# Kernel tuning notes

Hardware: AMD Instinct MI355X
Metric: run time of the kernel (lower is better)

Reference implementation:

```python
import jax, jax.numpy as jnp
import numpy as np

LLR_CLIP = 20.0   # allowed_llr_range(abs=20)
QMAX = 7.5        # decoder_qms_qbit = 5 -> round(x*2)/2, clip +/-7.5


def _quantize_ste(x):
    # straight-through quantizer: forward = quantized, grad flows through clipped x
    q = jnp.clip(jnp.round(x * 2.0) / 2.0, -QMAX, QMAX)
    xc = jnp.clip(x, -QMAX, QMAX)
    return xc + jax.lax.stop_gradient(q - xc)


def _decode(xa, cn_weights, vn_idx, cn_idx, shifts, M):
    # xa: (B, Z, N) channel LLRs; messages live on lifted edges (B, Z, E)
    B, Z, N = xa.shape
    E = vn_idx.shape[0]
    iters = cn_weights.shape[0]

    zidx = jnp.arange(Z)
    lift = (zidx[:, None] + shifts[None, :]) % Z    # VN-domain -> CN-domain cyclic shift per edge
    unlift = (zidx[:, None] - shifts[None, :]) % Z  # inverse shift
    lift_b = jnp.broadcast_to(lift[None], (B, Z, E))
    unlift_b = jnp.broadcast_to(unlift[None], (B, Z, E))

    V = jax.nn.one_hot(vn_idx, N, dtype=xa.dtype)   # (E, N) edge->VN incidence (= W_output / W_skipconn2even)
    eids = jnp.arange(E)
    llr_e = xa[:, :, vn_idx]                        # per-edge channel LLR (B, Z, E)

    c2v = jnp.zeros((B, Z, E), xa.dtype)
    for it in range(iters):
        # --- VN update (odd layer): extrinsic sum + channel LLR, clipped ---
        tot = jnp.einsum('bze,en->bzn', c2v, V)                 # per-VN sum of incoming c2v
        v2c = jnp.clip(llr_e + tot[:, :, vn_idx] - c2v, -LLR_CLIP, LLR_CLIP)

        # --- lift to CN domain (Lift_Matrix1) ---
        m = jnp.take_along_axis(v2c, lift_b, axis=1)            # (B, Z, E)
        mt = m.transpose(2, 0, 1).reshape(E, B * Z)             # edges leading for segment ops

        # --- CN update (even layer): extrinsic min-sum via two-min trick ---
        a = jnp.abs(mt)
        neg = (mt < 0).astype(jnp.int32)
        min1 = jax.ops.segment_min(a, cn_idx, num_segments=M)               # (M, B*Z)
        ismin = a == min1[cn_idx]
        first = jax.ops.segment_min(jnp.where(ismin, eids[:, None], E),
                                    cn_idx, num_segments=M)                 # tie-break by edge id
        isfirst = eids[:, None] == first[cn_idx]
        min2 = jax.ops.segment_min(jnp.where(isfirst, jnp.inf, a),
                                   cn_idx, num_segments=M)
        ext_min = jnp.where(isfirst, min2[cn_idx], min1[cn_idx])
        negtot = jax.ops.segment_sum(neg, cn_idx, num_segments=M)
        sgn = (1 - 2 * ((negtot[cn_idx] - neg) % 2)).astype(mt.dtype)       # extrinsic sign product

        msg = _quantize_ste(cn_weights[it] * sgn * ext_min)     # per-iteration scalar CN weight + QMS quantize

        # --- unlift back to VN domain (Lift_Matrix2) ---
        mc = msg.reshape(E, B, Z).transpose(1, 2, 0)
        c2v = jnp.take_along_axis(mc, unlift_b, axis=1)

    # marginal output LLRs (W_output): channel + all incoming c2v, shape (B, N*Z)
    out = xa + jnp.einsum('bze,en->bzn', c2v, V)
    return out.transpose(0, 2, 1).reshape(B, N * Z)


def setup_inputs() -> dict:
    key = jax.random.key(0)
    B, Z, N, M, dc = 32, 384, 68, 46, 7
    E = M * dc  # 322
    k1, k2, k3 = jax.random.split(key, 3)
    xa = jax.random.normal(k1, (B, Z, N), dtype=jnp.float32) * 4.0
    cn_weights = jnp.ones((8,), jnp.float32)
    cn_idx = jnp.repeat(jnp.arange(M), dc)                      # regular CN degree 7
    vn_idx = jax.random.randint(k2, (E,), 0, N)
    shifts = jax.random.randint(k3, (E,), 0, Z)
    return {"xa": xa, "cn_weights": cn_weights, "vn_idx": vn_idx,
            "cn_idx": cn_idx, "shifts": shifts, "M": M}


def reference(xa, cn_weights, vn_idx, cn_idx, shifts, M):
    return _decode(xa, cn_weights, vn_idx, cn_idx, shifts, M)
```

## Files before the change

kernel.cpp:

```cpp
#include <hip/hip_runtime.h>

#define B_   32
#define Z_   384
#define N_   68
#define M_   46
#define DC_  7
#define E_   (M_ * DC_)
#define ZN   (Z_ * N_)
#define ZM   (Z_ * M_)
#define Z2   768
#define MAXDV 20

#define PLZ(j,m) (((j) * M_ + (m)) * Z2)
#define ZT    (DC_ * M_ * Z2)
#define MS2S  (ZT + 1152)
#define CST2  154
#define OST   21

#define W2_XAT  0
#define XAT2I   (B_ * N_ * Z2)
#define MS2I    (B_ * MS2S / 4)
#define W2_MSG0 (W2_XAT + XAT2I)
#define W2_MSG1 (W2_MSG0 + MS2I)
#define W2_CHK  (W2_MSG1 + MS2I)
#define W2_OUT  (W2_CHK + M_ * CST2)
#define W2_END  (W2_OUT + N_ * OST)


__global__ __launch_bounds__(384)
void k_pre(const float* __restrict__ xa,
           const int* __restrict__ vn_idx, const int* __restrict__ shifts,
           int* __restrict__ ws)
{
    const int tid = threadIdx.x;
    if (blockIdx.x == B_ * 6) {
        __shared__ int vnl[E_], shl[E_], cntS[N_], posS[N_], offsS[N_ + 1], lstS[E_];
        if (tid < E_) { vnl[tid] = vn_idx[tid]; shl[tid] = shifts[tid]; }
        if (tid < N_) { cntS[tid] = 0; posS[tid] = 0; }
        __syncthreads();
        if (tid < E_) atomicAdd(&cntS[vnl[tid]], 1);
        __syncthreads();
        if (tid == 0) {
            offsS[0] = 0;
            for (int n = 0; n < N_; ++n) offsS[n + 1] = offsS[n] + cntS[n];
        }
        __syncthreads();
        if (tid < E_) {
            int m = tid / DC_, j = tid - m * DC_;
            int vn = vnl[tid];
            int r = atomicAdd(&posS[vn], 1);
            lstS[offsS[vn] + r] = (PLZ(j, m) << 9) | shl[tid];
        }
        __syncthreads();
        if (tid < E_) {
            int m = tid / DC_, j = tid - m * DC_;
            int vn = vnl[tid], sj = shl[tid];
            int* rec = ws + W2_CHK + m * CST2;
            rec[j] = vn * Z2 + sj;
            int o = offsS[vn];
            int dv = cntS[vn]; if (dv > MAXDV) dv = MAXDV;
            rec[7 + j] = (dv > 8) ? dv - 8 : 0;
            for (int q = 0; q < 8; ++q) {
                int slot = ZT;
                if (q < dv) {
                    int lr = lstS[o + q];
                    int sc = sj - (lr & 511); if (sc < 0) sc += Z_;
                    slot = (lr >> 9) + sc;
                }
                rec[14 + j * 8 + q] = slot;
            }
            for (int q = 8; q < dv; ++q) {
                int lr = lstS[o + q];
                int sc = sj - (lr & 511); if (sc < 0) sc += Z_;
                rec[70 + j * 12 + (q - 8)] = (lr >> 9) + sc;
            }
        }
        if (tid < N_) {
            int* rr = ws + W2_OUT + tid * OST;
            int o = offsS[tid];
            int dv = cntS[tid]; if (dv > MAXDV) dv = MAXDV;
            rr[8] = (dv > 8) ? dv - 8 : 0;
            for (int q = 0; q < 8; ++q) {
                int slot = ZT;
                if (q < dv) { int lr = lstS[o + q]; slot = (lr >> 9) + (Z_ - (lr & 511)); }
                rr[q] = slot;
            }
            for (int q = 8; q < dv; ++q) {
                int lr = lstS[o + q];
                rr[9 + (q - 8)] = (lr >> 9) + (Z_ - (lr & 511));
            }
        }
        return;
    }
    __shared__ float tile[N_ * 65];
    const int x = blockIdx.x & 7;
    const int k = blockIdx.x >> 3;
    const int b = x + 8 * (k & 3);
    const int t = k >> 2;
    const int z0 = t * 64;
    const float* src = xa + (size_t)b * ZN + (size_t)z0 * N_;
    for (int i = tid; i < 64 * N_; i += 384) {
        int r = i / N_, n = i - r * N_;
        tile[n * 65 + r] = src[i];
    }
    {
        int* t0 = ws + W2_MSG0 + (b * MS2S + ZT) / 4;
        int* t1 = ws + W2_MSG1 + (b * MS2S + ZT) / 4;
        if (tid < 48) t0[t * 48 + tid] = 0;
        else if (tid < 96) t1[t * 48 + (tid - 48)] = 0;
    }
    __syncthreads();
    float* dst = (float*)(ws + W2_XAT) + (size_t)b * N_ * Z2;
    for (int i = tid; i < 64 * N_; i += 384) {
        int n = i >> 6, zl = i & 63;
        float v = tile[n * 65 + zl];
        dst[n * Z2 + z0 + zl] = v;
        dst[n * Z2 + z0 + zl + Z_] = v;
    }
}

template <bool INIT>
__global__ __launch_bounds__(384)
void k_fit(const float* __restrict__ cw, const int* __restrict__ ws,
           const signed char* __restrict__ mold, signed char* __restrict__ mnew,
           int it)
{
    const int tid = threadIdx.x;
    const int bid = blockIdx.x;
    const int b = (bid & 7) + 8 * ((bid >> 3) & 3);
    const int tile = bid >> 5;
    const int z = tid;
    const float* xb = (const float*)(ws + W2_XAT) + (size_t)b * N_ * Z2;
    const signed char* mo = mold + (size_t)b * MS2S;
    signed char* mn = mnew + (size_t)b * MS2S;
    const float w = cw[it];

    for (int s = 0; s < 2; ++s) {
        const int m = 2 * tile + s;
        const int* tb = ws + W2_CHK + m * CST2;
        float m1 = 1e30f, m2v = 1e30f;
        int f = 0, negb = 0;
        #pragma unroll
        for (int j = 0; j < DC_; ++j) {
            float v = xb[tb[j] + z];
            if (!INIT) {
                int t2 = 0;
                #pragma unroll
                for (int q = 0; q < 8; ++q)
                    t2 += (int)mo[tb[14 + j * 8 + q] + z];
                const int dvx = tb[7 + j];
                for (int q = 0; q < dvx; ++q)
                    t2 += (int)mo[tb[70 + j * 12 + q] + z];
                const int c2 = (int)mo[PLZ(j, m) + z];
                float lt = v + 0.5f * (float)t2;
                v = lt - 0.5f * (float)c2;
            }
            v = fminf(fmaxf(v, -20.0f), 20.0f);
            negb |= (v < 0.0f) << j;
            float a = fabsf(v);
            if (a < m1) { m2v = m1; m1 = a; f = j; }
            else if (a < m2v) { m2v = a; }
        }
        float r1 = fminf(fmaxf(rintf(w * m1 * 2.0f), -15.0f), 15.0f);
        float r2 = fminf(fmaxf(rintf(w * m2v * 2.0f), -15.0f), 15.0f);
        const int q1 = (int)r1, q2 = (int)r2;
        const int par = __popc(negb);
        #pragma unroll
        for (int j = 0; j < DC_; ++j) {
            int q = (j == f) ? q2 : q1;
            int sj = (par - ((negb >> j) & 1)) & 1;
            signed char qv = (signed char)(sj ? -q : q);
            mn[PLZ(j, m) + z] = qv;
            mn[PLZ(j, m) + Z_ + z] = qv;
        }
    }
}

__global__ __launch_bounds__(384)
void k_out(const int* __restrict__ ws, const signed char* __restrict__ msg,
           float* __restrict__ dst)
{
    const int tid = threadIdx.x;
    const int bid = blockIdx.x;
    const int b = (bid & 7) + 8 * ((bid >> 3) & 3);
    const int kk = bid >> 5;
    const int z = tid;
    const signed char* mb = msg + (size_t)b * MS2S;
    const float* xb = (const float*)(ws + W2_XAT) + (size_t)b * N_ * Z2;
    for (int s = 0; s < 2; ++s) {
        const int n = 2 * kk + s;
        const int* rr = ws + W2_OUT + n * OST;
        int t2 = 0;
        #pragma unroll
        for (int q = 0; q < 8; ++q)
            t2 += (int)mb[rr[q] + z];
        const int dvx = rr[8];
        for (int q = 0; q < dvx; ++q)
            t2 += (int)mb[rr[9 + q] + z];
        dst[(size_t)b * ZN + n * Z_ + z] = xb[n * Z2 + z] + 0.5f * (float)t2;
    }
}

__global__ __launch_bounds__(384)
void k_tr(const float* __restrict__ xa, float* __restrict__ dst_g)
{
    __shared__ float tile[N_ * 65];
    const int tid = threadIdx.x;
    const int x = blockIdx.x & 7;
    const int k = blockIdx.x >> 3;
    const int b = x + 8 * (k & 3);
    const int t = k >> 2;
    const int z0 = t * 64;
    const float* src = xa + (size_t)b * ZN + (size_t)z0 * N_;
    for (int i = tid; i < 64 * N_; i += 384) {
        int r = i / N_, n = i - r * N_;
        tile[n * 65 + r] = src[i];
    }
    __syncthreads();
    float* dst = dst_g + (size_t)b * ZN + z0;
    for (int i = tid; i < 64 * N_; i += 384) {
        int n = i >> 6, zl = i & 63;
        dst[n * Z_ + zl] = tile[n * 65 + zl];
    }
}

#define INIT_STATE ((16u << 10) | (16u << 15))
__device__ __forceinline__ int decode2(unsigned st, int j) {
    int neg   = (st >> j) & 1;
    int q1    = (int)((st >> 10) & 31) - 16;
    int q2    = (int)((st >> 15) & 31) - 16;
    int first = (int)((st >> 7) & 7);
    int q     = (j == first) ? q2 : q1;
    int par   = (__popc(st & 127u) - neg) & 1;
    return par ? -q : q;
}

__global__ __launch_bounds__(1024)
void ldpc_decode_kernel(const float* __restrict__ xa,
                        const float* __restrict__ cw,
                        const int*   __restrict__ vn_idx,
                        const int*   __restrict__ shifts,
                        float* out, int iters)
{
    __shared__ short tot[ZN];
    __shared__ int   evs[E_];
    __shared__ int   offs[N_ + 1];
    __shared__ int   lists[E_];
    __shared__ float wlds[8];

    const int tid = threadIdx.x;
    const int b   = blockIdx.x;
    const float* xab = xa + (size_t)b * ZN;
    float* outb = out + (size_t)b * ZN;
    int* stateg = (int*)outb;

    if (tid < E_) evs[tid] = vn_idx[tid] | (shifts[tid] << 7);
    if (tid < iters && tid < 8) wlds[tid] = cw[tid];
    __syncthreads();
    if (tid < N_) {
        int c = 0;
        for (int e = 0; e < E_; ++e) c += ((evs[e] & 127) == tid);
        offs[tid + 1] = c;
    }
    if (tid == 0) offs[0] = 0;
    __syncthreads();
    if (tid == 0) { for (int n = 0; n < N_; ++n) offs[n + 1] += offs[n]; }
    __syncthreads();
    if (tid < N_) {
        int p = offs[tid];
        for (int e = 0; e < E_; ++e) {
            int rec = evs[e];
            if ((rec & 127) == tid) {
                int s = rec >> 7;
                lists[p++] = s | ((e / DC_) << 9) | ((e % DC_) << 15);
            }
        }
    }
    __syncthreads();

    for (int i = tid; i < ZM; i += 1024) stateg[i] = (int)INIT_STATE;
    __syncthreads();

    for (int it = 0; it < iters; ++it) {
        for (int i = tid; i < ZN; i += 1024) {
            int z = i / N_, n = i - z * N_, t2 = 0;
            int kend = offs[n + 1];
            for (int k = offs[n]; k < kend; ++k) {
                int rec = lists[k];
                int s = rec & 511, m = (rec >> 9) & 63, j = rec >> 15;
                int zs = z - s; if (zs < 0) zs += Z_;
                t2 += decode2((unsigned)stateg[zs * M_ + m], j);
            }
            tot[i] = (short)t2;
        }
        __syncthreads();
        const float w = wlds[it];
        for (int i = tid; i < ZM; i += 1024) {
            int z = i / M_, m = i - z * M_;
            unsigned st = (unsigned)stateg[i];
            float m1 = 1e30f, m2 = 1e30f;
            int f = 0, negb = 0;
            #pragma unroll
            for (int j = 0; j < DC_; ++j) {
                int rec = evs[m * DC_ + j];
                int vn = rec & 127, s = rec >> 7;
                int zr = z + s; if (zr >= Z_) zr -= Z_;
                int c2 = decode2(st, j);
                int idx = zr * N_ + vn;
                float v = (xab[idx] + 0.5f * (float)tot[idx]) - 0.5f * (float)c2;
                v = fminf(fmaxf(v, -20.0f), 20.0f);
                negb |= (v < 0.0f) << j;
                float a = fabsf(v);
                if (a < m1) { m2 = m1; m1 = a; f = j; }
                else if (a < m2) { m2 = a; }
            }
            float r1 = fminf(fmaxf(rintf(w * m1 * 2.0f), -15.0f), 15.0f);
            float r2 = fminf(fmaxf(rintf(w * m2 * 2.0f), -15.0f), 15.0f);
            stateg[i] = (int)(unsigned)(negb | (f << 7) | (((int)r1 + 16) << 10) | (((int)r2 + 16) << 15));
        }
        __syncthreads();
    }

    for (int i = tid; i < ZN; i += 1024) {
        int z = i / N_, n = i - z * N_, t2 = 0;
        int kend = offs[n + 1];
        for (int k = offs[n]; k < kend; ++k) {
            int rec = lists[k];
            int s = rec & 511, m = (rec >> 9) & 63, j = rec >> 15;
            int zs = z - s; if (zs < 0) zs += Z_;
            t2 += decode2((unsigned)stateg[zs * M_ + m], j);
        }
        tot[i] = (short)t2;
    }
    __syncthreads();
    for (int i = tid; i < ZN; i += 1024) {
        int n = i / Z_, z = i - n * Z_;
        outb[i] = xab[z * N_ + n] + 0.5f * (float)tot[z * N_ + n];
    }
}

extern "C" void kernel_launch(void* const* d_in, const int* in_sizes, int n_in,
                              void* d_out, int out_size, void* d_ws, size_t ws_size,
                              hipStream_t stream) {
    const float* xa = (const float*)d_in[0];
    const float* cw = (const float*)d_in[1];
    const int* vn   = (const int*)d_in[2];
    const int* sh   = (const int*)d_in[4];
    int iters = in_sizes[1];
    float* outp = (float*)d_out;

    if (ws_size >= (size_t)W2_END * sizeof(int)) {
        int*         ws   = (int*)d_ws;
        signed char* msg0 = (signed char*)(ws + W2_MSG0);
        signed char* msg1 = (signed char*)(ws + W2_MSG1);

        if (iters == 0) {
            hipLaunchKernelGGL(k_tr, dim3(B_ * 6), dim3(384), 0, stream, xa, outp);
            return;
        }
        hipLaunchKernelGGL(k_pre, dim3(B_ * 6 + 1), dim3(384), 0, stream,
                           xa, vn, sh, ws);
        hipLaunchKernelGGL((k_fit<true>), dim3(B_ * 23), dim3(384), 0, stream,
                           cw, ws, msg0, msg0, 0);
        for (int it = 1; it < iters; ++it) {
            signed char* wbuf = (it & 1) ? msg1 : msg0;
            signed char* rbuf = (it & 1) ? msg0 : msg1;
            hipLaunchKernelGGL((k_fit<false>), dim3(B_ * 23), dim3(384), 0, stream,
                               cw, ws, rbuf, wbuf, it);
        }
        signed char* fin = ((iters - 1) & 1) ? msg1 : msg0;
        hipLaunchKernelGGL(k_out, dim3(B_ * 34), dim3(384), 0, stream,
                           ws, fin, outp);
    } else {
        hipLaunchKernelGGL(ldpc_decode_kernel, dim3(B_), dim3(1024), 0, stream,
                           xa, cw, vn, sh, outp, iters);
    }
}
```

Before: 173.5 us.

## Pack four int8 messages per thread and stage check tables in shared memory

Measured after the change: 212.4 us. +22.4%, slower.

```diff
diff --git a/kernel.cpp b/kernel.cpp
--- a/kernel.cpp
+++ b/kernel.cpp
@@ -14,7 +14,7 @@
 #define PLZ(j,m) (((j) * M_ + (m)) * Z2)
 #define ZT    (DC_ * M_ * Z2)
 #define MS2S  (ZT + 1152)
-#define CST2  154
+#define CST3  154
 #define OST   21
 
 #define W2_XAT  0
@@ -23,7 +23,7 @@
 #define W2_MSG0 (W2_XAT + XAT2I)
 #define W2_MSG1 (W2_MSG0 + MS2I)
 #define W2_CHK  (W2_MSG1 + MS2I)
-#define W2_OUT  (W2_CHK + M_ * CST2)
+#define W2_OUT  (W2_CHK + M_ * CST3)
 #define W2_END  (W2_OUT + N_ * OST)
 
 
@@ -55,24 +55,15 @@
         if (tid < E_) {
             int m = tid / DC_, j = tid - m * DC_;
             int vn = vnl[tid], sj = shl[tid];
-            int* rec = ws + W2_CHK + m * CST2;
+            int* rec = ws + W2_CHK + m * CST3;
             rec[j] = vn * Z2 + sj;
             int o = offsS[vn];
             int dv = cntS[vn]; if (dv > MAXDV) dv = MAXDV;
-            rec[7 + j] = (dv > 8) ? dv - 8 : 0;
-            for (int q = 0; q < 8; ++q) {
-                int slot = ZT;
-                if (q < dv) {
-                    int lr = lstS[o + q];
-                    int sc = sj - (lr & 511); if (sc < 0) sc += Z_;
-                    slot = (lr >> 9) + sc;
-                }
-                rec[14 + j * 8 + q] = slot;
-            }
-            for (int q = 8; q < dv; ++q) {
+            rec[7 + j] = dv;
+            for (int q = 0; q < dv; ++q) {
                 int lr = lstS[o + q];
                 int sc = sj - (lr & 511); if (sc < 0) sc += Z_;
-                rec[70 + j * 12 + (q - 8)] = (lr >> 9) + sc;
+                rec[14 + j * 20 + q] = (lr >> 9) + sc;
             }
         }
         if (tid < N_) {
@@ -125,54 +116,88 @@
            const signed char* __restrict__ mold, signed char* __restrict__ mnew,
            int it)
 {
+    __shared__ int tbl[4 * CST3];
     const int tid = threadIdx.x;
     const int bid = blockIdx.x;
     const int b = (bid & 7) + 8 * ((bid >> 3) & 3);
     const int tile = bid >> 5;
-    const int z = tid;
+    for (int i = tid; i < 4 * CST3; i += 384) {
+        int mm = tile * 4 + i / CST3;
+        if (mm < M_) tbl[i] = ws[W2_CHK + mm * CST3 + (i - (i / CST3) * CST3)];
+    }
+    __syncthreads();
+    const int c = tid / 96;
+    const int g = tid - 96 * c;
+    const int m = tile * 4 + c;
+    if (m >= M_) return;
+    const int zb = 4 * g;
+    const int* tb = &tbl[c * CST3];
     const float* xb = (const float*)(ws + W2_XAT) + (size_t)b * N_ * Z2;
-    const signed char* mo = mold + (size_t)b * MS2S;
-    signed char* mn = mnew + (size_t)b * MS2S;
+    const unsigned* mo4 = (const unsigned*)(mold + (size_t)b * MS2S);
+    unsigned* mn4 = (unsigned*)(mnew + (size_t)b * MS2S);
     const float w = cw[it];
 
-    for (int s = 0; s < 2; ++s) {
-        const int m = 2 * tile + s;
-        const int* tb = ws + W2_CHK + m * CST2;
-        float m1 = 1e30f, m2v = 1e30f;
-        int f = 0, negb = 0;
+    float m1[4], m2[4];
+    int f[4], ng[4];
+    #pragma unroll
+    for (int k = 0; k < 4; ++k) { m1[k] = 1e30f; m2[k] = 1e30f; f[k] = 0; ng[k] = 0; }
+
+    #pragma unroll
+    for (int j = 0; j < DC_; ++j) {
+        const int lb = tb[j] + zb;
+        float vv[4];
         #pragma unroll
-        for (int j = 0; j < DC_; ++j) {
-            float v = xb[tb[j] + z];
-            if (!INIT) {
-                int t2 = 0;
+        for (int k = 0; k < 4; ++k) vv[k] = xb[lb + k];
+        if (!INIT) {
+            int t2[4] = {0, 0, 0, 0};
+            const int dv = tb[7 + j];
+            for (int q = 0; q < dv; ++q) {
+                const int a = tb[14 + j * 20 + q] + zb;
+                const int a0 = a >> 2;
+                const int r = (a & 3) * 8;
+                unsigned w0 = mo4[a0], w1 = mo4[a0 + 1];
+                unsigned long long dw = ((unsigned long long)w1 << 32) | w0;
+                unsigned packed = (unsigned)(dw >> r);
                 #pragma unroll
-                for (int q = 0; q < 8; ++q)
-                    t2 += (int)mo[tb[14 + j * 8 + q] + z];
-                const int dvx = tb[7 + j];
-                for (int q = 0; q < dvx; ++q)
-                    t2 += (int)mo[tb[70 + j * 12 + q] + z];
-                const int c2 = (int)mo[PLZ(j, m) + z];
-                float lt = v + 0.5f * (float)t2;
-                v = lt - 0.5f * (float)c2;
-            }
-            v = fminf(fmaxf(v, -20.0f), 20.0f);
-            negb |= (v < 0.0f) << j;
+                for (int k = 0; k < 4; ++k)
+                    t2[k] += (int)(signed char)(packed >> (8 * k));
+            }
+            const unsigned ow = mo4[(PLZ(j, m) + zb) >> 2];
+            #pragma unroll
+            for (int k = 0; k < 4; ++k) {
+                int c2 = (int)(signed char)(ow >> (8 * k));
+                float lt = vv[k] + 0.5f * (float)t2[k];
+                vv[k] = lt - 0.5f * (float)c2;
+            }
+        }
+        #pragma unroll
+        for (int k = 0; k < 4; ++k) {
+            float v = fminf(fmaxf(vv[k], -20.0f), 20.0f);
+            ng[k] |= (v < 0.0f) << j;
             float a = fabsf(v);
-            if (a < m1) { m2v = m1; m1 = a; f = j; }
-            else if (a < m2v) { m2v = a; }
-        }
-        float r1 = fminf(fmaxf(rintf(w * m1 * 2.0f), -15.0f), 15.0f);
-        float r2 = fminf(fmaxf(rintf(w * m2v * 2.0f), -15.0f), 15.0f);
-        const int q1 = (int)r1, q2 = (int)r2;
-        const int par = __popc(negb);
+            if (a < m1[k]) { m2[k] = m1[k]; m1[k] = a; f[k] = j; }
+            else if (a < m2[k]) { m2[k] = a; }
+        }
+    }
+    int q1[4], q2[4], par[4];
+    #pragma unroll
+    for (int k = 0; k < 4; ++k) {
+        float r1 = fminf(fmaxf(rintf(w * m1[k] * 2.0f), -15.0f), 15.0f);
+        float r2 = fminf(fmaxf(rintf(w * m2[k] * 2.0f), -15.0f), 15.0f);
+        q1[k] = (int)r1; q2[k] = (int)r2; par[k] = __popc(ng[k]);
+    }
+    #pragma unroll
+    for (int j = 0; j < DC_; ++j) {
+        unsigned outw = 0;
         #pragma unroll
-        for (int j = 0; j < DC_; ++j) {
-            int q = (j == f) ? q2 : q1;
-            int sj = (par - ((negb >> j) & 1)) & 1;
-            signed char qv = (signed char)(sj ? -q : q);
-            mn[PLZ(j, m) + z] = qv;
-            mn[PLZ(j, m) + Z_ + z] = qv;
-        }
+        for (int k = 0; k < 4; ++k) {
+            int q = (j == f[k]) ? q2[k] : q1[k];
+            int sj = (par[k] - ((ng[k] >> j) & 1)) & 1;
+            outw |= ((unsigned)((sj ? -q : q) & 0xff)) << (8 * k);
+        }
+        const int base = PLZ(j, m) + zb;
+        mn4[base >> 2] = outw;
+        mn4[(base + Z_) >> 2] = outw;
     }
 }
 
@@ -360,12 +385,12 @@
         }
         hipLaunchKernelGGL(k_pre, dim3(B_ * 6 + 1), dim3(384), 0, stream,
                            xa, vn, sh, ws);
-        hipLaunchKernelGGL((k_fit<true>), dim3(B_ * 23), dim3(384), 0, stream,
+        hipLaunchKernelGGL((k_fit<true>), dim3(B_ * 12), dim3(384), 0, stream,
                            cw, ws, msg0, msg0, 0);
         for (int it = 1; it < iters; ++it) {
             signed char* wbuf = (it & 1) ? msg1 : msg0;
             signed char* rbuf = (it & 1) ? msg0 : msg1;
-            hipLaunchKernelGGL((k_fit<false>), dim3(B_ * 23), dim3(384), 0, stream,
+            hipLaunchKernelGGL((k_fit<false>), dim3(B_ * 12), dim3(384), 0, stream,
                                cw, ws, rbuf, wbuf, it);
         }
         signed char* fin = ((iters - 1) & 1) ? msg1 : msg0;
```

## Fuse preprocessing and first check-node iteration into one per-batch kernel

Applied to the files above, without the earlier changes.

Result: slower. 214.3 us (+23.5%).

```diff
diff --git a/kernel.cpp b/kernel.cpp
--- a/kernel.cpp
+++ b/kernel.cpp
@@ -14,7 +14,7 @@
 #define PLZ(j,m) (((j) * M_ + (m)) * Z2)
 #define ZT    (DC_ * M_ * Z2)
 #define MS2S  (ZT + 1152)
-#define CST2  154
+#define CST3  154
 #define OST   21
 
 #define W2_XAT  0
@@ -23,17 +23,17 @@
 #define W2_MSG0 (W2_XAT + XAT2I)
 #define W2_MSG1 (W2_MSG0 + MS2I)
 #define W2_CHK  (W2_MSG1 + MS2I)
-#define W2_OUT  (W2_CHK + M_ * CST2)
+#define W2_OUT  (W2_CHK + M_ * CST3)
 #define W2_END  (W2_OUT + N_ * OST)
 
 
 __global__ __launch_bounds__(384)
-void k_pre(const float* __restrict__ xa,
-           const int* __restrict__ vn_idx, const int* __restrict__ shifts,
-           int* __restrict__ ws)
+void k_init0(const float* __restrict__ xa, const float* __restrict__ cw,
+             const int* __restrict__ vn_idx, const int* __restrict__ shifts,
+             int* __restrict__ ws)
 {
     const int tid = threadIdx.x;
-    if (blockIdx.x == B_ * 6) {
+    if (blockIdx.x == B_) {
         __shared__ int vnl[E_], shl[E_], cntS[N_], posS[N_], offsS[N_ + 1], lstS[E_];
         if (tid < E_) { vnl[tid] = vn_idx[tid]; shl[tid] = shifts[tid]; }
         if (tid < N_) { cntS[tid] = 0; posS[tid] = 0; }
@@ -55,7 +55,7 @@
         if (tid < E_) {
             int m = tid / DC_, j = tid - m * DC_;
             int vn = vnl[tid], sj = shl[tid];
-            int* rec = ws + W2_CHK + m * CST2;
+            int* rec = ws + W2_CHK + m * CST3;
             rec[j] = vn * Z2 + sj;
             int o = offsS[vn];
             int dv = cntS[vn]; if (dv > MAXDV) dv = MAXDV;
@@ -92,34 +92,63 @@
         }
         return;
     }
-    __shared__ float tile[N_ * 65];
-    const int x = blockIdx.x & 7;
-    const int k = blockIdx.x >> 3;
-    const int b = x + 8 * (k & 3);
-    const int t = k >> 2;
-    const int z0 = t * 64;
-    const float* src = xa + (size_t)b * ZN + (size_t)z0 * N_;
-    for (int i = tid; i < 64 * N_; i += 384) {
-        int r = i / N_, n = i - r * N_;
-        tile[n * 65 + r] = src[i];
-    }
+
+    __shared__ float lds[Z_ * 69];
+    __shared__ int evn[E_];
+    __shared__ int esh[E_];
+    const int b = blockIdx.x;
+    const float* src = xa + (size_t)b * ZN;
+    for (int i = tid; i < ZN; i += 384) {
+        int zz = i / N_, nn = i - zz * N_;
+        lds[zz * 69 + nn] = src[i];
+    }
+    if (tid < E_) { evn[tid] = vn_idx[tid]; esh[tid] = shifts[tid]; }
     {
         int* t0 = ws + W2_MSG0 + (b * MS2S + ZT) / 4;
         int* t1 = ws + W2_MSG1 + (b * MS2S + ZT) / 4;
-        if (tid < 48) t0[t * 48 + tid] = 0;
-        else if (tid < 96) t1[t * 48 + (tid - 48)] = 0;
-    }
-    __syncthreads();
+        if (tid < 288) { t0[tid] = 0; t1[tid] = 0; }
+    }
+    __syncthreads();
+
+    const int z = tid;
     float* dst = (float*)(ws + W2_XAT) + (size_t)b * N_ * Z2;
-    for (int i = tid; i < 64 * N_; i += 384) {
-        int n = i >> 6, zl = i & 63;
-        float v = tile[n * 65 + zl];
-        dst[n * Z2 + z0 + zl] = v;
-        dst[n * Z2 + z0 + zl + Z_] = v;
-    }
-}
-
-template <bool INIT>
+    for (int n = 0; n < N_; ++n) {
+        float v = lds[z * 69 + n];
+        dst[n * Z2 + z] = v;
+        dst[n * Z2 + z + Z_] = v;
+    }
+
+    const float w = cw[0];
+    signed char* mn = (signed char*)(ws + W2_MSG0) + (size_t)b * MS2S;
+    for (int m = 0; m < M_; ++m) {
+        float m1 = 1e30f, m2v = 1e30f;
+        int f = 0, negb = 0;
+        #pragma unroll
+        for (int j = 0; j < DC_; ++j) {
+            const int e = m * DC_ + j;
+            int zr = z + esh[e]; if (zr >= Z_) zr -= Z_;
+            float v = lds[zr * 69 + evn[e]];
+            v = fminf(fmaxf(v, -20.0f), 20.0f);
+            negb |= (v < 0.0f) << j;
+            float a = fabsf(v);
+            if (a < m1) { m2v = m1; m1 = a; f = j; }
+            else if (a < m2v) { m2v = a; }
+        }
+        float r1 = fminf(fmaxf(rintf(w * m1 * 2.0f), -15.0f), 15.0f);
+        float r2 = fminf(fmaxf(rintf(w * m2v * 2.0f), -15.0f), 15.0f);
+        const int q1 = (int)r1, q2 = (int)r2;
+        const int par = __popc(negb);
+        #pragma unroll
+        for (int j = 0; j < DC_; ++j) {
+            int q = (j == f) ? q2 : q1;
+            int sj = (par - ((negb >> j) & 1)) & 1;
+            signed char qv = (signed char)(sj ? -q : q);
+            mn[PLZ(j, m) + z] = qv;
+            mn[PLZ(j, m) + Z_ + z] = qv;
+        }
+    }
+}
+
 __global__ __launch_bounds__(384)
 void k_fit(const float* __restrict__ cw, const int* __restrict__ ws,
            const signed char* __restrict__ mold, signed char* __restrict__ mnew,
@@ -135,15 +164,16 @@
     signed char* mn = mnew + (size_t)b * MS2S;
     const float w = cw[it];
 
+    #pragma unroll
     for (int s = 0; s < 2; ++s) {
         const int m = 2 * tile + s;
-        const int* tb = ws + W2_CHK + m * CST2;
+        const int* tb = ws + W2_CHK + m * CST3;
         float m1 = 1e30f, m2v = 1e30f;
         int f = 0, negb = 0;
         #pragma unroll
         for (int j = 0; j < DC_; ++j) {
             float v = xb[tb[j] + z];
-            if (!INIT) {
+            {
                 int t2 = 0;
                 #pragma unroll
                 for (int q = 0; q < 8; ++q)
@@ -187,6 +217,7 @@
     const int z = tid;
     const signed char* mb = msg + (size_t)b * MS2S;
     const float* xb = (const float*)(ws + W2_XAT) + (size_t)b * N_ * Z2;
+    #pragma unroll
     for (int s = 0; s < 2; ++s) {
         const int n = 2 * kk + s;
         const int* rr = ws + W2_OUT + n * OST;
@@ -358,14 +389,12 @@
             hipLaunchKernelGGL(k_tr, dim3(B_ * 6), dim3(384), 0, stream, xa, outp);
             return;
         }
-        hipLaunchKernelGGL(k_pre, dim3(B_ * 6 + 1), dim3(384), 0, stream,
-                           xa, vn, sh, ws);
-        hipLaunchKernelGGL((k_fit<true>), dim3(B_ * 23), dim3(384), 0, stream,
-                           cw, ws, msg0, msg0, 0);
+        hipLaunchKernelGGL(k_init0, dim3(B_ + 1), dim3(384), 0, stream,
+                           xa, cw, vn, sh, ws);
         for (int it = 1; it < iters; ++it) {
             signed char* wbuf = (it & 1) ? msg1 : msg0;
             signed char* rbuf = (it & 1) ? msg0 : msg1;
-            hipLaunchKernelGGL((k_fit<false>), dim3(B_ * 23), dim3(384), 0, stream,
+            hipLaunchKernelGGL(k_fit, dim3(B_ * 23), dim3(384), 0, stream,
                                cw, ws, rbuf, wbuf, it);
         }
         signed char* fin = ((iters - 1) & 1) ? msg1 : msg0;
```
